# Kernel optimization log

Hardware: AMD Instinct MI355X
Metric: run time of the kernel (lower is better)

Reference implementation:

```python
import jax, jax.numpy as jnp
import numpy as np

D_MODEL = 1024
N_HEADS = 16
D_FF = 4096
LN_EPS = 1e-5


def _layer_norm(x, g, b):
    m = jnp.mean(x, axis=-1, keepdims=True)
    v = jnp.mean((x - m) ** 2, axis=-1, keepdims=True)
    return (x - m) / jnp.sqrt(v + LN_EPS) * g + b


def setup_inputs() -> dict:
    key = jax.random.key(0)
    ks = jax.random.split(key, 16)
    s = 0.02
    d, dff = D_MODEL, D_FF
    return {
        "x": jax.random.normal(ks[0], (8, 1000, d), dtype=jnp.float32),
        # weights stored as (d_in, d_out); applied via x @ W
        "wq": jax.random.normal(ks[1], (d, d), dtype=jnp.float32) * s,
        "wk": jax.random.normal(ks[2], (d, d), dtype=jnp.float32) * s,
        "wv": jax.random.normal(ks[3], (d, d), dtype=jnp.float32) * s,
        "wo": jax.random.normal(ks[4], (d, d), dtype=jnp.float32) * s,
        "bo": jnp.zeros((d,), dtype=jnp.float32),
        "w1": jax.random.normal(ks[5], (d, dff), dtype=jnp.float32) * s,
        "b1": jnp.zeros((dff,), dtype=jnp.float32),
        "w2": jax.random.normal(ks[6], (dff, d), dtype=jnp.float32) * s,
        "b2": jnp.zeros((d,), dtype=jnp.float32),
        "g1": jnp.ones((d,), dtype=jnp.float32),
        "beta1": jnp.zeros((d,), dtype=jnp.float32),
        "g2": jnp.ones((d,), dtype=jnp.float32),
        "beta2": jnp.zeros((d,), dtype=jnp.float32),
    }


def reference(x, wq, wk, wv, wo, bo, w1, b1, w2, b2, g1, beta1, g2, beta2):
    B, S, D = x.shape
    H = N_HEADS
    dk = D // H

    # --- pre-norm attention ---
    h = _layer_norm(x, g1, beta1)
    q = (h @ wq).reshape(B, S, H, dk)
    k = (h @ wk).reshape(B, S, H, dk)
    v = (h @ wv).reshape(B, S, H, dk)
    scores = jnp.einsum('bqhd,bkhd->bhqk', q, k) / jnp.sqrt(jnp.float32(dk))
    mask = jnp.tril(jnp.ones((S, S), dtype=bool))  # causal
    scores = jnp.where(mask, scores, -jnp.inf)
    attn = jax.nn.softmax(scores, axis=-1)
    attended = jnp.einsum('bhqk,bkhd->bqhd', attn, v).reshape(B, S, D)
    x = x + attended @ wo + bo

    # --- pre-norm FFN (exact GELU, matching torch F.gelu default) ---
    h2 = _layer_norm(x, g2, beta2)
    ff = jax.nn.gelu(h2 @ w1 + b1, approximate=False) @ w2 + b2
    return x + ff
```

## Files before the change

kernel.cpp:

```cpp
#include <hip/hip_runtime.h>
#include <hip/hip_bf16.h>
#include <math.h>

#define D_MODEL 1024
#define D_FF    4096
#define N_HEADS 16
#define SEQ     1000
#define BATCH   8
#define M_TOK   (BATCH * SEQ)

typedef __bf16 bf16x8_t __attribute__((ext_vector_type(8)));
typedef short  short8_t __attribute__((ext_vector_type(8)));
typedef float  f32x4_t  __attribute__((ext_vector_type(4)));

__device__ __forceinline__ f32x4_t mfma_bf16(short8_t a, short8_t b, f32x4_t c) {
    return __builtin_amdgcn_mfma_f32_16x16x32_bf16(
        __builtin_bit_cast(bf16x8_t, a), __builtin_bit_cast(bf16x8_t, b), c, 0, 0, 0);
}

__device__ __forceinline__ unsigned short f2bf(float f) {
    union { float f; unsigned u; } x; x.f = f;
    unsigned r = (x.u + 0x7fffu + ((x.u >> 16) & 1u)) >> 16;
    return (unsigned short)r;
}

__device__ __forceinline__ float gelu_fast(float v) {
    float z = 1.5957691216f * v * fmaf(0.044715f, v * v, 1.0f);
    float e = __expf(-z);
    return v * __builtin_amdgcn_rcpf(1.0f + e);
}

__device__ __forceinline__ void gload_lds16(const void* g, void* l) {
    __builtin_amdgcn_global_load_lds(
        (const __attribute__((address_space(1))) unsigned int*)g,
        (__attribute__((address_space(3))) unsigned int*)l, 16, 0, 0);
}

__global__ __launch_bounds__(256) void prep_kernel(
    const float* __restrict__ wq, const float* __restrict__ wk,
    const float* __restrict__ wv, const float* __restrict__ wo,
    const float* __restrict__ w1, const float* __restrict__ w2,
    unsigned short* __restrict__ wqt, unsigned short* __restrict__ wkt,
    unsigned short* __restrict__ wvt, unsigned short* __restrict__ wot,
    unsigned short* __restrict__ w1t, unsigned short* __restrict__ w2t,
    const float* __restrict__ x, const float* __restrict__ g1,
    const float* __restrict__ beta1, unsigned short* __restrict__ h1) {
    int id = blockIdx.x;
    __shared__ float tile[32][33];
    __shared__ float red[8];
    if (id >= 12288) {
        int row = id - 12288, tid = threadIdx.x;
        const float4 v = ((const float4*)(x + (size_t)row * D_MODEL))[tid];
        float s  = v.x + v.y + v.z + v.w;
        float s2 = v.x * v.x + v.y * v.y + v.z * v.z + v.w * v.w;
#pragma unroll
        for (int o = 32; o > 0; o >>= 1) { s += __shfl_xor(s, o, 64); s2 += __shfl_xor(s2, o, 64); }
        int wave = tid >> 6, lane = tid & 63;
        if (lane == 0) { red[wave] = s; red[wave + 4] = s2; }
        __syncthreads();
        s  = red[0] + red[1] + red[2] + red[3];
        s2 = red[4] + red[5] + red[6] + red[7];
        float mean = s * (1.0f / D_MODEL);
        float var  = s2 * (1.0f / D_MODEL) - mean * mean;
        float rstd = rsqrtf(var + 1e-5f);
        float4 gg = ((const float4*)g1)[tid];
        float4 bb = ((const float4*)beta1)[tid];
        ushort4 o4;
        o4.x = f2bf((v.x - mean) * rstd * gg.x + bb.x);
        o4.y = f2bf((v.y - mean) * rstd * gg.y + bb.y);
        o4.z = f2bf((v.z - mean) * rstd * gg.z + bb.z);
        o4.w = f2bf((v.w - mean) * rstd * gg.w + bb.w);
        ((ushort4*)(h1 + (size_t)row * D_MODEL))[tid] = o4;
        return;
    }
    const float* w; unsigned short* wt; int Kd, Nd, bx, by;
    if (id < 4096) {
        int z = id >> 10, t = id & 1023;
        w  = z == 0 ? wq  : z == 1 ? wk  : z == 2 ? wv  : wo;
        wt = z == 0 ? wqt : z == 1 ? wkt : z == 2 ? wvt : wot;
        Kd = 1024; Nd = 1024; bx = t & 31; by = t >> 5;
    } else if (id < 8192) {
        int t = id - 4096;
        w = w1; wt = w1t; Kd = 1024; Nd = 4096; bx = t & 127; by = t >> 7;
    } else {
        int t = id - 8192;
        w = w2; wt = w2t; Kd = 4096; Nd = 1024; bx = t & 31; by = t >> 5;
    }
    int n0 = bx * 32, k0 = by * 32;
    int tx = threadIdx.x & 31, ty = threadIdx.x >> 5;
#pragma unroll
    for (int i = 0; i < 4; ++i)
        tile[ty + i * 8][tx] = w[(size_t)(k0 + ty + i * 8) * Nd + n0 + tx];
    __syncthreads();
#pragma unroll
    for (int i = 0; i < 4; ++i)
        wt[(size_t)(n0 + ty + i * 8) * Kd + k0 + tx] = f2bf(tile[tx][ty + i * 8]);
}

__global__ __launch_bounds__(256) void vtrans_kernel(const unsigned short* __restrict__ v,
                                                     unsigned short* __restrict__ vt) {
    __shared__ unsigned short tile[32][33];
    int b = blockIdx.z;
    int c0 = blockIdx.x * 32, s0 = blockIdx.y * 32;
    int tx = threadIdx.x, ty = threadIdx.y;
#pragma unroll
    for (int i = 0; i < 4; ++i) {
        int s = s0 + ty + i * 8;
        unsigned short val = 0;
        if (s < SEQ) val = v[((size_t)b * SEQ + s) * D_MODEL + c0 + tx];
        tile[ty + i * 8][tx] = val;
    }
    __syncthreads();
#pragma unroll
    for (int i = 0; i < 4; ++i) {
        int c = c0 + ty + i * 8;
        vt[((size_t)b * D_MODEL + c) * 1024 + s0 + tx] = tile[tx][ty + i * 8];
    }
}

__global__ __launch_bounds__(256) void ln_kernel(const float* __restrict__ x,
                                                 const float* __restrict__ g,
                                                 const float* __restrict__ beta,
                                                 unsigned short* __restrict__ out) {
    int row = blockIdx.x, tid = threadIdx.x;
    const float4 v = ((const float4*)(x + (size_t)row * D_MODEL))[tid];
    float s  = v.x + v.y + v.z + v.w;
    float s2 = v.x * v.x + v.y * v.y + v.z * v.z + v.w * v.w;
#pragma unroll
    for (int o = 32; o > 0; o >>= 1) { s += __shfl_xor(s, o, 64); s2 += __shfl_xor(s2, o, 64); }
    __shared__ float red[8];
    int wave = tid >> 6, lane = tid & 63;
    if (lane == 0) { red[wave] = s; red[wave + 4] = s2; }
    __syncthreads();
    s  = red[0] + red[1] + red[2] + red[3];
    s2 = red[4] + red[5] + red[6] + red[7];
    float mean = s * (1.0f / D_MODEL);
    float var  = s2 * (1.0f / D_MODEL) - mean * mean;
    float rstd = rsqrtf(var + 1e-5f);
    float4 gg = ((const float4*)g)[tid];
    float4 bb = ((const float4*)beta)[tid];
    ushort4 o4;
    o4.x = f2bf((v.x - mean) * rstd * gg.x + bb.x);
    o4.y = f2bf((v.y - mean) * rstd * gg.y + bb.y);
    o4.z = f2bf((v.z - mean) * rstd * gg.z + bb.z);
    o4.w = f2bf((v.w - mean) * rstd * gg.w + bb.w);
    ((ushort4*)(out + (size_t)row * D_MODEL))[tid] = o4;
}

enum { EPI_BF16 = 0, EPI_GELU = 1, EPI_RES_F32 = 2 };

template <int EPI, bool FUSE3>
__global__ __launch_bounds__(512, 2) void gemm256(
    const unsigned short* __restrict__ A,
    const unsigned short* __restrict__ Bt0,
    const unsigned short* __restrict__ Bt1,
    const unsigned short* __restrict__ Bt2,
    const float* __restrict__ bias,
    const float* __restrict__ resid,
    void* __restrict__ out0, void* out1, void* out2,
    int Mdim, int Ndim, int K) {
    __shared__ unsigned short lds[4][2][256 * 32];
    int tid = threadIdx.x;
    int lane = tid & 63, wave = tid >> 6;
    int l15 = lane & 15, quad = lane >> 4;
    int wr = wave >> 2;
    int wc = wave & 3;
    int rt = blockIdx.y * 256;
    const unsigned short* Bt = Bt0;
    void* outp = out0;
    int ct;
    if (FUSE3) {
        int sel = blockIdx.x >> 2;
        ct = (blockIdx.x & 3) * 256;
        Bt   = sel == 0 ? Bt0  : (sel == 1 ? Bt1  : Bt2);
        outp = sel == 0 ? out0 : (sel == 1 ? out1 : out2);
    } else {
        ct = blockIdx.x * 256;
    }

    const unsigned short* aS[2];
    const unsigned short* bS[2];
#pragma unroll
    for (int j = 0; j < 2; ++j) {
        int gl = tid + j * 512;
        int p = gl >> 3, slot = gl & 7;
        int sp = slot ^ (p & 7);
        int rrow = 2 * p + (sp >> 2), g2 = sp & 3;
        int ar = rt + rrow; if (ar >= Mdim) ar = Mdim - 1;
        aS[j] = A  + (size_t)ar * K + g2 * 8;
        bS[j] = Bt + (size_t)(ct + rrow) * K + g2 * 8;
    }
    auto stageA = [&](int kt) {
        char* base = (char*)&lds[kt & 3][0][0];
#pragma unroll
        for (int j = 0; j < 2; ++j)
            gload_lds16(aS[j] + (size_t)kt * 32, base + (wave * 64 + j * 512) * 16);
    };
    auto stageB = [&](int kt) {
        char* base = (char*)&lds[kt & 3][1][0];
#pragma unroll
        for (int j = 0; j < 2; ++j)
            gload_lds16(bS[j] + (size_t)kt * 32, base + (wave * 64 + j * 512) * 16);
    };

    int lh = l15 >> 1;
    int mslot = (quad + ((l15 & 1) << 2)) ^ lh;
    unsigned aOff = (unsigned)((wr * 64 + lh) * 128 + mslot * 16);
    unsigned bOff = (unsigned)((wc * 32 + lh) * 128 + mslot * 16);

    f32x4_t acc[8][4] = {};
    int NT = K >> 5;

    stageA(0); stageB(0); stageA(1); stageB(1); stageA(2); stageB(2);

    for (int t = 0; t < NT; ++t) {
        int sl = t & 3;
        int rem = NT - 1 - t;
        if (rem >= 2)      asm volatile("s_waitcnt vmcnt(8)" ::: "memory");
        else if (rem == 1) asm volatile("s_waitcnt vmcnt(4)" ::: "memory");
        else               asm volatile("s_waitcnt vmcnt(0)" ::: "memory");
        __builtin_amdgcn_s_barrier();
        const char* la = (const char*)&lds[sl][0][0];
        const char* lb = (const char*)&lds[sl][1][0];
        short8_t af[4], bfv[4];
#pragma unroll
        for (int mi = 0; mi < 4; ++mi)
            af[mi] = *(const short8_t*)(la + aOff + mi * 1024);
#pragma unroll
        for (int ni = 0; ni < 4; ++ni)
            bfv[ni] = *(const short8_t*)(lb + bOff + ni * 1024);
        if (t + 3 < NT) stageA(t + 3);
        __builtin_amdgcn_s_setprio(1);
#pragma unroll
        for (int mi = 0; mi < 4; ++mi)
#pragma unroll
            for (int ni = 0; ni < 4; ++ni)
                acc[mi][ni] = mfma_bf16(af[mi], bfv[ni], acc[mi][ni]);
        __builtin_amdgcn_s_setprio(0);
        asm volatile("" ::: "memory");
        __builtin_amdgcn_s_barrier();
#pragma unroll
        for (int mi = 0; mi < 4; ++mi)
            af[mi] = *(const short8_t*)(la + aOff + 4096 + mi * 1024);
        if (t + 3 < NT) stageB(t + 3);
        __builtin_amdgcn_s_setprio(1);
#pragma unroll
        for (int mi = 0; mi < 4; ++mi)
#pragma unroll
            for (int ni = 0; ni < 4; ++ni)
                acc[4 + mi][ni] = mfma_bf16(af[mi], bfv[ni], acc[4 + mi][ni]);
        __builtin_amdgcn_s_setprio(0);
    }

    float bias_c[4];
    if (EPI != EPI_BF16) {
#pragma unroll
        for (int ni = 0; ni < 4; ++ni) bias_c[ni] = bias[ct + wc * 64 + ni * 16 + l15];
    }

#pragma unroll
    for (int mi = 0; mi < 8; ++mi) {
#pragma unroll
        for (int r = 0; r < 4; ++r) {
            int grow = rt + wr * 128 + mi * 16 + quad * 4 + r;
            if (grow >= Mdim) continue;
#pragma unroll
            for (int ni = 0; ni < 4; ++ni) {
                int gcol = ct + wc * 64 + ni * 16 + l15;
                float v = acc[mi][ni][r];
                size_t idx = (size_t)grow * Ndim + gcol;
                if (EPI == EPI_BF16) {
                    ((unsigned short*)outp)[idx] = f2bf(v);
                } else if (EPI == EPI_GELU) {
                    v += bias_c[ni];
                    ((unsigned short*)outp)[idx] = f2bf(gelu_fast(v));
                } else {
                    v += bias_c[ni] + resid[idx];
                    ((float*)outp)[idx] = v;
                }
            }
        }
    }
}

template <int EPI, bool FUSE3>
__global__ __launch_bounds__(512, 2) void gemm128(
    const unsigned short* __restrict__ A,
    const unsigned short* __restrict__ Bt0,
    const unsigned short* __restrict__ Bt1,
    const unsigned short* __restrict__ Bt2,
    const float* __restrict__ bias,
    const float* __restrict__ resid,
    void* __restrict__ out0, void* out1, void* out2,
    int Mdim, int Ndim, int K) {
    __shared__ unsigned short ldsA[4][128 * 32];
    __shared__ unsigned short ldsB[4][256 * 32];
    int tid = threadIdx.x;
    int lane = tid & 63, wave = tid >> 6;
    int l15 = lane & 15, quad = lane >> 4;
    int wr = wave >> 2;
    int wc = wave & 3;
    int rt = blockIdx.y * 128;
    const unsigned short* Bt = Bt0;
    void* outp = out0;
    int ct;
    if (FUSE3) {
        int sel = blockIdx.x >> 2;
        ct = (blockIdx.x & 3) * 256;
        Bt   = sel == 0 ? Bt0  : (sel == 1 ? Bt1  : Bt2);
        outp = sel == 0 ? out0 : (sel == 1 ? out1 : out2);
    } else {
        ct = blockIdx.x * 256;
    }

    const unsigned short* aSrc;
    {
        int p = tid >> 3, sp = (tid & 7) ^ (p & 7);
        int rrow = 2 * p + (sp >> 2), g2 = sp & 3;
        int ar = rt + rrow; if (ar >= Mdim) ar = Mdim - 1;
        aSrc = A + (size_t)ar * K + g2 * 8;
    }
    const unsigned short* bSrc[2];
#pragma unroll
    for (int j = 0; j < 2; ++j) {
        int gl = tid + j * 512;
        int p = gl >> 3, sp = (gl & 7) ^ (p & 7);
        int rrow = 2 * p + (sp >> 2), g2 = sp & 3;
        bSrc[j] = Bt + (size_t)(ct + rrow) * K + g2 * 8;
    }
    auto stage = [&](int kt) {
        int sl = kt & 3;
        gload_lds16(aSrc + (size_t)kt * 32, (char*)ldsA[sl] + wave * 1024);
        gload_lds16(bSrc[0] + (size_t)kt * 32, (char*)ldsB[sl] + wave * 1024);
        gload_lds16(bSrc[1] + (size_t)kt * 32, (char*)ldsB[sl] + 8192 + wave * 1024);
    };

    int lh = l15 >> 1;
    int mslot = (quad + ((l15 & 1) << 2)) ^ lh;
    unsigned aOff = (unsigned)((wr * 32 + lh) * 128 + mslot * 16);
    unsigned bOff = (unsigned)((wc * 32 + lh) * 128 + mslot * 16);

    f32x4_t acc[4][4] = {};
    int NT = K >> 5;

    stage(0); stage(1); stage(2);

    for (int t = 0; t < NT; ++t) {
        int sl = t & 3;
        int rem = NT - 1 - t;
        if (rem >= 2)      asm volatile("s_waitcnt vmcnt(6)" ::: "memory");
        else if (rem == 1) asm volatile("s_waitcnt vmcnt(3)" ::: "memory");
        else               asm volatile("s_waitcnt vmcnt(0)" ::: "memory");
        __builtin_amdgcn_s_barrier();
        const char* la = (const char*)ldsA[sl];
        const char* lb = (const char*)ldsB[sl];
        short8_t af[4], bfv[4];
#pragma unroll
        for (int mi = 0; mi < 4; ++mi)
            af[mi] = *(const short8_t*)(la + aOff + mi * 1024);
#pragma unroll
        for (int ni = 0; ni < 4; ++ni)
            bfv[ni] = *(const short8_t*)(lb + bOff + ni * 1024);
        if (t + 3 < NT) stage(t + 3);
        __builtin_amdgcn_s_setprio(1);
#pragma unroll
        for (int mi = 0; mi < 4; ++mi)
#pragma unroll
            for (int ni = 0; ni < 4; ++ni)
                acc[mi][ni] = mfma_bf16(af[mi], bfv[ni], acc[mi][ni]);
        __builtin_amdgcn_s_setprio(0);
    }

    float bias_c[4];
    if (EPI != EPI_BF16) {
#pragma unroll
        for (int ni = 0; ni < 4; ++ni) bias_c[ni] = bias[ct + wc * 64 + ni * 16 + l15];
    }

#pragma unroll
    for (int mi = 0; mi < 4; ++mi) {
#pragma unroll
        for (int r = 0; r < 4; ++r) {
            int grow = rt + wr * 64 + mi * 16 + quad * 4 + r;
            if (grow >= Mdim) continue;
#pragma unroll
            for (int ni = 0; ni < 4; ++ni) {
                int gcol = ct + wc * 64 + ni * 16 + l15;
                float v = acc[mi][ni][r];
                size_t idx = (size_t)grow * Ndim + gcol;
                if (EPI == EPI_BF16) {
                    ((unsigned short*)outp)[idx] = f2bf(v);
                } else if (EPI == EPI_GELU) {
                    v += bias_c[ni];
                    ((unsigned short*)outp)[idx] = f2bf(gelu_fast(v));
                } else {
                    v += bias_c[ni] + resid[idx];
                    ((float*)outp)[idx] = v;
                }
            }
        }
    }
}

__global__ __launch_bounds__(256) void attn_kernel(
    const unsigned short* __restrict__ q,
    const unsigned short* __restrict__ k,
    const unsigned short* __restrict__ vt,
    unsigned short* __restrict__ att) {
    int p = blockIdx.x, h = blockIdx.y, b = blockIdx.z;
    int tid = threadIdx.x, lane = tid & 63, wave = tid >> 6;
    int l15 = lane & 15, quad = lane >> 4;
    __shared__ unsigned short kt_lds[2][64 * 64];
    __shared__ unsigned short vt_lds[2][64 * 64];
    __shared__ unsigned short p_lds[4][32 * 64];
    unsigned short* pw = p_lds[wave];

    const int qtA = p, qtB = 7 - p;
    const int tA = 2 * qtA + 2, tB = 2 * qtB + 2, total = tA + tB;

    short8_t aq[2][2][2];
#pragma unroll
    for (int ph = 0; ph < 2; ++ph) {
        int qw = (ph ? qtB : qtA) * 128 + wave * 32;
#pragma unroll
        for (int g = 0; g < 2; ++g) {
            int qr = qw + g * 16 + l15; if (qr > SEQ - 1) qr = SEQ - 1;
            const unsigned short* qp = q + ((size_t)(b * SEQ + qr)) * D_MODEL + h * 64 + quad * 8;
            aq[ph][g][0] = *(const short8_t*)qp;
            aq[ph][g][1] = *(const short8_t*)(qp + 32);
        }
    }

    f32x4_t o[2][4] = {};
    float m_run[2] = {-3.0e38f, -3.0e38f};
    float l_run[2] = {0.f, 0.f};

    auto stage = [&](int kt, int bufi) {
#pragma unroll
        for (int i = 0; i < 2; ++i) {
            int g2 = tid + i * 256;
            int row = g2 >> 3, cp = g2 & 7;
            int c = cp ^ (row & 7);
            int key = kt * 64 + row; int keyc = key < SEQ ? key : SEQ - 1;
            gload_lds16(k + ((size_t)(b * SEQ + keyc)) * D_MODEL + h * 64 + c * 8,
                        (char*)kt_lds[bufi] + (size_t)(wave * 64 + i * 256) * 16);
            gload_lds16(vt + ((size_t)((b * N_HEADS + h) * 64 + row)) * 1024 + kt * 64 + c * 8,
                        (char*)vt_lds[bufi] + (size_t)(wave * 64 + i * 256) * 16);
        }
    };

    auto flush = [&](int qt) {
#pragma unroll
        for (int g = 0; g < 2; ++g) {
            float linv = __builtin_amdgcn_rcpf(l_run[g]);
#pragma unroll
            for (int r = 0; r < 4; ++r) {
                float nr = __shfl(linv, quad * 4 + r, 64);
                int qg = qt * 128 + wave * 32 + g * 16 + quad * 4 + r;
                if (qg >= SEQ) continue;
#pragma unroll
                for (int db = 0; db < 4; ++db)
                    att[((size_t)(b * SEQ + qg)) * D_MODEL + h * 64 + db * 16 + l15] =
                        f2bf(o[g][db][r] * nr);
            }
        }
#pragma unroll
        for (int g = 0; g < 2; ++g) {
            m_run[g] = -3.0e38f; l_run[g] = 0.f;
#pragma unroll
            for (int db = 0; db < 4; ++db) o[g][db] = f32x4_t{0.f, 0.f, 0.f, 0.f};
        }
    };

    stage(0, 0);

    for (int i = 0; i < total; ++i) {
        int bufi = i & 1;
        __syncthreads();
        if (i + 1 < total) {
            int nkt = (i + 1 < tA) ? (i + 1) : (i + 1 - tA);
            stage(nkt, bufi ^ 1);
        }
        int phase = (i < tA) ? 0 : 1;
        int kt = (i < tA) ? i : i - tA;
        int qt = phase ? qtB : qtA;
        int qw = qt * 128 + wave * 32;
        const unsigned short* kl = kt_lds[bufi];
        const unsigned short* vl = vt_lds[bufi];

        if (kt * 64 <= qw + 31) {
            short8_t kf[4][2];
#pragma unroll
            for (int nb = 0; nb < 4; ++nb)
#pragma unroll
                for (int kc = 0; kc < 2; ++kc) {
                    int row = nb * 16 + l15;
                    kf[nb][kc] = *(const short8_t*)(kl + (row * 8 + ((kc * 4 + quad) ^ (row & 7))) * 8);
                }

            bool gact[2];
#pragma unroll
            for (int g = 0; g < 2; ++g) {
                gact[g] = (kt * 64 <= qw + g * 16 + 15);
                if (!gact[g]) continue;
                f32x4_t s[4] = {};
#pragma unroll
                for (int nb = 0; nb < 4; ++nb)
#pragma unroll
                    for (int kc = 0; kc < 2; ++kc)
                        s[nb] = mfma_bf16(kf[nb][kc], aq[phase][g][kc], s[nb]);
                int qrow = qw + g * 16 + l15;
                float sc[4][4];
#pragma unroll
                for (int nb = 0; nb < 4; ++nb)
#pragma unroll
                    for (int r = 0; r < 4; ++r) {
                        int key = kt * 64 + nb * 16 + quad * 4 + r;
                        float v = s[nb][r] * 0.125f;
                        sc[nb][r] = (key <= qrow) ? v : -1e30f;
                    }
                float mx = sc[0][0];
#pragma unroll
                for (int nb = 0; nb < 4; ++nb)
#pragma unroll
                    for (int r = 0; r < 4; ++r) mx = fmaxf(mx, sc[nb][r]);
                mx = fmaxf(mx, __shfl_xor(mx, 16, 64));
                mx = fmaxf(mx, __shfl_xor(mx, 32, 64));
                float mnew = fmaxf(m_run[g], mx);
                float alpha = __expf(m_run[g] - mnew);
                m_run[g] = mnew;
                float rs = 0.f;
#pragma unroll
                for (int nb = 0; nb < 4; ++nb)
#pragma unroll
                    for (int r = 0; r < 4; ++r) {
                        float pv = __expf(sc[nb][r] - mnew);
                        sc[nb][r] = pv;
                        rs += pv;
                    }
                rs += __shfl_xor(rs, 16, 64);
                rs += __shfl_xor(rs, 32, 64);
                l_run[g] = l_run[g] * alpha + rs;
#pragma unroll
                for (int r = 0; r < 4; ++r) {
                    float a = __shfl(alpha, quad * 4 + r, 64);
#pragma unroll
                    for (int db = 0; db < 4; ++db) o[g][db][r] *= a;
                }
#pragma unroll
                for (int nb = 0; nb < 4; ++nb) {
                    unsigned long long pv =
                        (unsigned long long)f2bf(sc[nb][0]) |
                        ((unsigned long long)f2bf(sc[nb][1]) << 16) |
                        ((unsigned long long)f2bf(sc[nb][2]) << 32) |
                        ((unsigned long long)f2bf(sc[nb][3]) << 48);
                    int chunk = (4 * nb + quad) ^ ((l15 & 7) << 1);
                    *(unsigned long long*)(pw + (g * 16 + l15) * 64 + chunk * 4) = pv;
                }
            }
            asm volatile("s_waitcnt lgkmcnt(0)" ::: "memory");

            short8_t vf[4][2];
#pragma unroll
            for (int db = 0; db < 4; ++db)
#pragma unroll
                for (int kc = 0; kc < 2; ++kc) {
                    int row = db * 16 + l15;
                    vf[db][kc] = *(const short8_t*)(vl + (row * 8 + ((kc * 4 + quad) ^ (row & 7))) * 8);
                }
#pragma unroll
            for (int g = 0; g < 2; ++g) {
                if (!gact[g]) continue;
                short8_t ap[2];
#pragma unroll
                for (int kc = 0; kc < 2; ++kc)
                    ap[kc] = *(const short8_t*)(pw + (g * 16 + l15) * 64 +
                                                ((kc * 4 + quad) ^ (l15 & 7)) * 8);
#pragma unroll
                for (int db = 0; db < 4; ++db)
#pragma unroll
                    for (int kc = 0; kc < 2; ++kc)
                        o[g][db] = mfma_bf16(ap[kc], vf[db][kc], o[g][db]);
            }
        }

        if (i == tA - 1) flush(qtA);
    }
    flush(qtB);
}

extern "C" void kernel_launch(void* const* d_in, const int* in_sizes, int n_in,
                              void* d_out, int out_size, void* d_ws, size_t ws_size,
                              hipStream_t stream) {
    const float* x     = (const float*)d_in[0];
    const float* wq    = (const float*)d_in[1];
    const float* wk    = (const float*)d_in[2];
    const float* wv    = (const float*)d_in[3];
    const float* wo    = (const float*)d_in[4];
    const float* bo    = (const float*)d_in[5];
    const float* w1    = (const float*)d_in[6];
    const float* b1    = (const float*)d_in[7];
    const float* w2    = (const float*)d_in[8];
    const float* b2    = (const float*)d_in[9];
    const float* g1    = (const float*)d_in[10];
    const float* beta1 = (const float*)d_in[11];
    const float* g2    = (const float*)d_in[12];
    const float* beta2 = (const float*)d_in[13];
    float* out = (float*)d_out;
    char* ws = (char*)d_ws;

    const size_t SZ_MD_BF16 = (size_t)M_TOK * D_MODEL * 2;
    unsigned short* h1  = (unsigned short*)(ws);
    unsigned short* qb  = (unsigned short*)(ws + SZ_MD_BF16);
    unsigned short* kb  = (unsigned short*)(ws + 2 * SZ_MD_BF16);
    unsigned short* vb  = (unsigned short*)(ws + 3 * SZ_MD_BF16);
    unsigned short* atb = (unsigned short*)(ws + 4 * SZ_MD_BF16);
    unsigned short* ffb = qb;
    size_t off = 5 * SZ_MD_BF16;
    unsigned short* vtb = (unsigned short*)(ws + off); off += (size_t)BATCH * D_MODEL * 1024 * 2;
    float* x1 = (float*)(ws + off); off += (size_t)M_TOK * D_MODEL * 4;
    unsigned short* wqt = (unsigned short*)(ws + off); off += (size_t)D_MODEL * D_MODEL * 2;
    unsigned short* wkt = (unsigned short*)(ws + off); off += (size_t)D_MODEL * D_MODEL * 2;
    unsigned short* wvt = (unsigned short*)(ws + off); off += (size_t)D_MODEL * D_MODEL * 2;
    unsigned short* wot = (unsigned short*)(ws + off); off += (size_t)D_MODEL * D_MODEL * 2;
    unsigned short* w1t = (unsigned short*)(ws + off); off += (size_t)D_MODEL * D_FF * 2;
    unsigned short* w2t = (unsigned short*)(ws + off); off += (size_t)D_MODEL * D_FF * 2;

    prep_kernel<<<12288 + M_TOK, 256, 0, stream>>>(
        wq, wk, wv, wo, w1, w2, wqt, wkt, wvt, wot, w1t, w2t, x, g1, beta1, h1);

    const int MT128 = (M_TOK + 127) / 128;
    const int MT256 = (M_TOK + 255) / 256;

    gemm128<EPI_BF16, true><<<dim3(12, MT128), 512, 0, stream>>>(
        h1, wqt, wkt, wvt, nullptr, nullptr, qb, kb, vb, M_TOK, D_MODEL, D_MODEL);

    dim3 tb(32, 8);
    vtrans_kernel<<<dim3(32, 32, 8), tb, 0, stream>>>(vb, vtb);

    attn_kernel<<<dim3(4, N_HEADS, BATCH), 256, 0, stream>>>(qb, kb, vtb, atb);

    gemm128<EPI_RES_F32, false><<<dim3(4, MT128), 512, 0, stream>>>(
        atb, wot, nullptr, nullptr, bo, x, x1, nullptr, nullptr, M_TOK, D_MODEL, D_MODEL);

    ln_kernel<<<M_TOK, 256, 0, stream>>>(x1, g2, beta2, h1);

    gemm256<EPI_GELU, false><<<dim3(16, MT256), 512, 0, stream>>>(
        h1, w1t, nullptr, nullptr, b1, nullptr, ffb, nullptr, nullptr, M_TOK, D_FF, D_MODEL);

    gemm128<EPI_RES_F32, false><<<dim3(4, MT128), 512, 0, stream>>>(
        ffb, w2t, nullptr, nullptr, b2, x1, out, nullptr, nullptr, M_TOK, D_MODEL, D_FF);
}
```

Measured before the change: 477.4 us.

## Add 256x256 GEMM with K=64 double buffering and four-phase interleaved pipeline

Replaces the 256-tile GEMM with a version that stages K=64 slices into two LDS buffers and splits each K step into four MFMA phases. Global-to-LDS loads for the next tiles are interleaved between phases, with explicit barriers and sched_barrier calls. The QKV projection moves from 128-row tiles to this 256-row kernel. The aim is to hide load latency and raise MFMA density on the large GEMMs, at the cost of more barriers and a 128KB LDS footprint, which lowers occupancy.

```diff
diff --git a/kernel.cpp b/kernel.cpp
--- a/kernel.cpp
+++ b/kernel.cpp
@@ -149,8 +149,8 @@
 
 enum { EPI_BF16 = 0, EPI_GELU = 1, EPI_RES_F32 = 2 };
 
-template <int EPI, bool FUSE3>
-__global__ __launch_bounds__(512, 2) void gemm256(
+template <int EPI, bool FUSE3, int SLOTS>
+__global__ __launch_bounds__(512, 2) void gemm128t(
     const unsigned short* __restrict__ A,
     const unsigned short* __restrict__ Bt0,
     const unsigned short* __restrict__ Bt1,
@@ -159,7 +159,134 @@
     const float* __restrict__ resid,
     void* __restrict__ out0, void* out1, void* out2,
     int Mdim, int Ndim, int K) {
-    __shared__ unsigned short lds[4][2][256 * 32];
+    constexpr int DIST = SLOTS - 1;
+    __shared__ unsigned short ldsA[SLOTS][128 * 32];
+    __shared__ unsigned short ldsB[SLOTS][256 * 32];
+    int tid = threadIdx.x;
+    int lane = tid & 63, wave = tid >> 6;
+    int l15 = lane & 15, quad = lane >> 4;
+    int wr = wave >> 2;
+    int wc = wave & 3;
+    int rt = blockIdx.y * 128;
+    const unsigned short* Bt = Bt0;
+    void* outp = out0;
+    int ct;
+    if (FUSE3) {
+        int sel = blockIdx.x >> 2;
+        ct = (blockIdx.x & 3) * 256;
+        Bt   = sel == 0 ? Bt0  : (sel == 1 ? Bt1  : Bt2);
+        outp = sel == 0 ? out0 : (sel == 1 ? out1 : out2);
+    } else {
+        ct = blockIdx.x * 256;
+    }
+
+    const unsigned short* aSrc;
+    {
+        int p = tid >> 3, sp = (tid & 7) ^ (p & 7);
+        int rrow = 2 * p + (sp >> 2), g2 = sp & 3;
+        int ar = rt + rrow; if (ar >= Mdim) ar = Mdim - 1;
+        aSrc = A + (size_t)ar * K + g2 * 8;
+    }
+    const unsigned short* bSrc[2];
+#pragma unroll
+    for (int j = 0; j < 2; ++j) {
+        int gl = tid + j * 512;
+        int p = gl >> 3, sp = (gl & 7) ^ (p & 7);
+        int rrow = 2 * p + (sp >> 2), g2 = sp & 3;
+        bSrc[j] = Bt + (size_t)(ct + rrow) * K + g2 * 8;
+    }
+    auto stage = [&](int kt, int sl) {
+        gload_lds16(aSrc + (size_t)kt * 32, (char*)ldsA[sl] + wave * 1024);
+        gload_lds16(bSrc[0] + (size_t)kt * 32, (char*)ldsB[sl] + wave * 1024);
+        gload_lds16(bSrc[1] + (size_t)kt * 32, (char*)ldsB[sl] + 8192 + wave * 1024);
+    };
+
+    int lh = l15 >> 1;
+    int mslot = (quad + ((l15 & 1) << 2)) ^ lh;
+    unsigned aOff = (unsigned)((wr * 32 + lh) * 128 + mslot * 16);
+    unsigned bOff = (unsigned)((wc * 32 + lh) * 128 + mslot * 16);
+
+    f32x4_t acc[4][4] = {};
+    int NT = K >> 5;
+
+#pragma unroll
+    for (int d = 0; d < DIST; ++d) stage(d, d);
+
+    int scur = 0, spre = DIST;
+    for (int t = 0; t < NT; ++t) {
+        int rem = NT - 1 - t;
+        if constexpr (SLOTS == 4) {
+            if (rem >= 2)      asm volatile("s_waitcnt vmcnt(6)" ::: "memory");
+            else if (rem == 1) asm volatile("s_waitcnt vmcnt(3)" ::: "memory");
+            else               asm volatile("s_waitcnt vmcnt(0)" ::: "memory");
+        } else {
+            if (rem >= 1)      asm volatile("s_waitcnt vmcnt(3)" ::: "memory");
+            else               asm volatile("s_waitcnt vmcnt(0)" ::: "memory");
+        }
+        __builtin_amdgcn_s_barrier();
+        const char* la = (const char*)ldsA[scur];
+        const char* lb = (const char*)ldsB[scur];
+        short8_t af[4], bfv[4];
+#pragma unroll
+        for (int mi = 0; mi < 4; ++mi)
+            af[mi] = *(const short8_t*)(la + aOff + mi * 1024);
+#pragma unroll
+        for (int ni = 0; ni < 4; ++ni)
+            bfv[ni] = *(const short8_t*)(lb + bOff + ni * 1024);
+        if (t + DIST < NT) stage(t + DIST, spre);
+        __builtin_amdgcn_s_setprio(1);
+#pragma unroll
+        for (int mi = 0; mi < 4; ++mi)
+#pragma unroll
+            for (int ni = 0; ni < 4; ++ni)
+                acc[mi][ni] = mfma_bf16(af[mi], bfv[ni], acc[mi][ni]);
+        __builtin_amdgcn_s_setprio(0);
+        scur = (scur == SLOTS - 1) ? 0 : scur + 1;
+        spre = (spre == SLOTS - 1) ? 0 : spre + 1;
+    }
+
+    float bias_c[4];
+    if (EPI != EPI_BF16) {
+#pragma unroll
+        for (int ni = 0; ni < 4; ++ni) bias_c[ni] = bias[ct + wc * 64 + ni * 16 + l15];
+    }
+
+#pragma unroll
+    for (int mi = 0; mi < 4; ++mi) {
+#pragma unroll
+        for (int r = 0; r < 4; ++r) {
+            int grow = rt + wr * 64 + mi * 16 + quad * 4 + r;
+            if (grow >= Mdim) continue;
+#pragma unroll
+            for (int ni = 0; ni < 4; ++ni) {
+                int gcol = ct + wc * 64 + ni * 16 + l15;
+                float v = acc[mi][ni][r];
+                size_t idx = (size_t)grow * Ndim + gcol;
+                if (EPI == EPI_BF16) {
+                    ((unsigned short*)outp)[idx] = f2bf(v);
+                } else if (EPI == EPI_GELU) {
+                    v += bias_c[ni];
+                    ((unsigned short*)outp)[idx] = f2bf(gelu_fast(v));
+                } else {
+                    v += bias_c[ni] + resid[idx];
+                    ((float*)outp)[idx] = v;
+                }
+            }
+        }
+    }
+}
+
+template <int EPI, bool FUSE3>
+__global__ __launch_bounds__(512, 2) void gemm256ph(
+    const unsigned short* __restrict__ A,
+    const unsigned short* __restrict__ Bt0,
+    const unsigned short* __restrict__ Bt1,
+    const unsigned short* __restrict__ Bt2,
+    const float* __restrict__ bias,
+    const float* __restrict__ resid,
+    void* __restrict__ out0, void* out1, void* out2,
+    int Mdim, int Ndim, int K) {
+    __shared__ unsigned short lds[2][32768];
     int tid = threadIdx.x;
     int lane = tid & 63, wave = tid >> 6;
     int l15 = lane & 15, quad = lane >> 4;
@@ -178,78 +305,137 @@
         ct = blockIdx.x * 256;
     }
 
-    const unsigned short* aS[2];
-    const unsigned short* bS[2];
+    int r6 = tid >> 3, s8 = tid & 7;
+    int gswA = (s8 ^ (r6 & 7)) * 8;
+    const unsigned short* aP[2][2];
+#pragma unroll
+    for (int j = 0; j < 2; ++j)
+#pragma unroll
+        for (int h = 0; h < 2; ++h) {
+            int ar = rt + j * 128 + h * 64 + r6;
+            if (ar >= Mdim) ar = Mdim - 1;
+            aP[j][h] = A + (size_t)ar * K + gswA;
+        }
+    const unsigned short* bP[2][2];
 #pragma unroll
     for (int j = 0; j < 2; ++j) {
-        int gl = tid + j * 512;
-        int p = gl >> 3, slot = gl & 7;
-        int sp = slot ^ (p & 7);
-        int rrow = 2 * p + (sp >> 2), g2 = sp & 3;
-        int ar = rt + rrow; if (ar >= Mdim) ar = Mdim - 1;
-        aS[j] = A  + (size_t)ar * K + g2 * 8;
-        bS[j] = Bt + (size_t)(ct + rrow) * K + g2 * 8;
-    }
-    auto stageA = [&](int kt) {
-        char* base = (char*)&lds[kt & 3][0][0];
-#pragma unroll
-        for (int j = 0; j < 2; ++j)
-            gload_lds16(aS[j] + (size_t)kt * 32, base + (wave * 64 + j * 512) * 16);
+        int G = tid + j * 512;
+        int q = G >> 8, idx = G & 255;
+        int r5 = idx >> 3, sb = idx & 7;
+        int gswB = (sb ^ (r5 & 7)) * 8;
+#pragma unroll
+        for (int h = 0; h < 2; ++h)
+            bP[j][h] = Bt + (size_t)(ct + q * 64 + h * 32 + r5) * K + gswB;
+    }
+    char* ldsb = (char*)lds;
+    int bwoff = (wave >> 2) * 8192 + (wave & 3) * 1024;
+    auto stA = [&](int kt, int h) {
+        char* d = ldsb + (size_t)(kt & 1) * 65536 + h * 8192 + wave * 1024;
+        gload_lds16(aP[0][h] + (size_t)kt * 64, d);
+        gload_lds16(aP[1][h] + (size_t)kt * 64, d + 16384);
     };
-    auto stageB = [&](int kt) {
-        char* base = (char*)&lds[kt & 3][1][0];
-#pragma unroll
-        for (int j = 0; j < 2; ++j)
-            gload_lds16(bS[j] + (size_t)kt * 32, base + (wave * 64 + j * 512) * 16);
+    auto stB = [&](int kt, int h) {
+        char* d = ldsb + (size_t)(kt & 1) * 65536 + 32768 + h * 4096 + bwoff;
+        gload_lds16(bP[0][h] + (size_t)kt * 64, d);
+        gload_lds16(bP[1][h] + (size_t)kt * 64, d + 16384);
     };
 
-    int lh = l15 >> 1;
-    int mslot = (quad + ((l15 & 1) << 2)) ^ lh;
-    unsigned aOff = (unsigned)((wr * 64 + lh) * 128 + mslot * 16);
-    unsigned bOff = (unsigned)((wc * 32 + lh) * 128 + mslot * 16);
+    unsigned sw0 = (unsigned)((quad ^ (l15 & 7)) * 16);
+    unsigned sw1 = sw0 ^ 64;
+    unsigned aB = (unsigned)(wr * 16384 + l15 * 128);
+    unsigned bB = (unsigned)(32768 + wc * 8192 + l15 * 128);
 
     f32x4_t acc[8][4] = {};
-    int NT = K >> 5;
-
-    stageA(0); stageB(0); stageA(1); stageB(1); stageA(2); stageB(2);
-
-    for (int t = 0; t < NT; ++t) {
-        int sl = t & 3;
-        int rem = NT - 1 - t;
-        if (rem >= 2)      asm volatile("s_waitcnt vmcnt(8)" ::: "memory");
-        else if (rem == 1) asm volatile("s_waitcnt vmcnt(4)" ::: "memory");
-        else               asm volatile("s_waitcnt vmcnt(0)" ::: "memory");
-        __builtin_amdgcn_s_barrier();
-        const char* la = (const char*)&lds[sl][0][0];
-        const char* lb = (const char*)&lds[sl][1][0];
-        short8_t af[4], bfv[4];
+    int NT = K >> 6;
+
+    stA(0, 0); stB(0, 0); stA(0, 1); stB(0, 1);
+    stA(1, 0); stB(1, 0); stA(1, 1);
+    asm volatile("s_waitcnt vmcnt(6)" ::: "memory");
+    __builtin_amdgcn_s_barrier();
+
+    short8_t af[4][2], bf[4][2];
+    for (int kt = 0; kt < NT; ++kt) {
+        const char* sbase = ldsb + (size_t)(kt & 1) * 65536;
+#pragma unroll
+        for (int mi = 0; mi < 4; ++mi) {
+            af[mi][0] = *(const short8_t*)(sbase + aB + sw0 + mi * 2048);
+            af[mi][1] = *(const short8_t*)(sbase + aB + sw1 + mi * 2048);
+        }
+#pragma unroll
+        for (int ni = 0; ni < 2; ++ni) {
+            bf[ni][0] = *(const short8_t*)(sbase + bB + sw0 + ni * 2048);
+            bf[ni][1] = *(const short8_t*)(sbase + bB + sw1 + ni * 2048);
+        }
+        if (kt + 1 < NT) stB(kt + 1, 1);
+        __builtin_amdgcn_s_barrier();
+        asm volatile("s_waitcnt lgkmcnt(0)" ::: "memory");
+        __builtin_amdgcn_sched_barrier(0);
+        __builtin_amdgcn_s_setprio(1);
 #pragma unroll
         for (int mi = 0; mi < 4; ++mi)
-            af[mi] = *(const short8_t*)(la + aOff + mi * 1024);
-#pragma unroll
-        for (int ni = 0; ni < 4; ++ni)
-            bfv[ni] = *(const short8_t*)(lb + bOff + ni * 1024);
-        if (t + 3 < NT) stageA(t + 3);
+#pragma unroll
+            for (int ni = 0; ni < 2; ++ni) {
+                acc[mi][ni] = mfma_bf16(af[mi][0], bf[ni][0], acc[mi][ni]);
+                acc[mi][ni] = mfma_bf16(af[mi][1], bf[ni][1], acc[mi][ni]);
+            }
+        __builtin_amdgcn_s_setprio(0);
+        __builtin_amdgcn_s_barrier();
+#pragma unroll
+        for (int ni = 2; ni < 4; ++ni) {
+            bf[ni][0] = *(const short8_t*)(sbase + bB + sw0 + ni * 2048);
+            bf[ni][1] = *(const short8_t*)(sbase + bB + sw1 + ni * 2048);
+        }
+        if (kt + 2 < NT) stA(kt + 2, 0);
+        __builtin_amdgcn_s_barrier();
+        asm volatile("s_waitcnt lgkmcnt(0)" ::: "memory");
+        __builtin_amdgcn_sched_barrier(0);
         __builtin_amdgcn_s_setprio(1);
 #pragma unroll
         for (int mi = 0; mi < 4; ++mi)
 #pragma unroll
-            for (int ni = 0; ni < 4; ++ni)
-                acc[mi][ni] = mfma_bf16(af[mi], bfv[ni], acc[mi][ni]);
+            for (int ni = 2; ni < 4; ++ni) {
+                acc[mi][ni] = mfma_bf16(af[mi][0], bf[ni][0], acc[mi][ni]);
+                acc[mi][ni] = mfma_bf16(af[mi][1], bf[ni][1], acc[mi][ni]);
+            }
         __builtin_amdgcn_s_setprio(0);
-        asm volatile("" ::: "memory");
-        __builtin_amdgcn_s_barrier();
+        __builtin_amdgcn_s_barrier();
+#pragma unroll
+        for (int mi = 0; mi < 4; ++mi) {
+            af[mi][0] = *(const short8_t*)(sbase + aB + sw0 + (mi + 4) * 2048);
+            af[mi][1] = *(const short8_t*)(sbase + aB + sw1 + (mi + 4) * 2048);
+        }
+        if (kt + 2 < NT) stB(kt + 2, 0);
+        __builtin_amdgcn_s_barrier();
+        asm volatile("s_waitcnt lgkmcnt(0)" ::: "memory");
+        __builtin_amdgcn_sched_barrier(0);
+        __builtin_amdgcn_s_setprio(1);
 #pragma unroll
         for (int mi = 0; mi < 4; ++mi)
-            af[mi] = *(const short8_t*)(la + aOff + 4096 + mi * 1024);
-        if (t + 3 < NT) stageB(t + 3);
+#pragma unroll
+            for (int ni = 2; ni < 4; ++ni) {
+                acc[mi + 4][ni] = mfma_bf16(af[mi][0], bf[ni][0], acc[mi + 4][ni]);
+                acc[mi + 4][ni] = mfma_bf16(af[mi][1], bf[ni][1], acc[mi + 4][ni]);
+            }
+        __builtin_amdgcn_s_setprio(0);
+        __builtin_amdgcn_s_barrier();
+        if (kt + 2 < NT) {
+            stA(kt + 2, 1);
+            asm volatile("s_waitcnt vmcnt(6)" ::: "memory");
+        } else {
+            asm volatile("s_waitcnt vmcnt(0)" ::: "memory");
+        }
+        __builtin_amdgcn_s_barrier();
+        __builtin_amdgcn_sched_barrier(0);
         __builtin_amdgcn_s_setprio(1);
 #pragma unroll
         for (int mi = 0; mi < 4; ++mi)
 #pragma unroll
-            for (int ni = 0; ni < 4; ++ni)
-                acc[4 + mi][ni] = mfma_bf16(af[mi], bfv[ni], acc[4 + mi][ni]);
+            for (int ni = 0; ni < 2; ++ni) {
+                acc[mi + 4][ni] = mfma_bf16(af[mi][0], bf[ni][0], acc[mi + 4][ni]);
+                acc[mi + 4][ni] = mfma_bf16(af[mi][1], bf[ni][1], acc[mi + 4][ni]);
+            }
         __builtin_amdgcn_s_setprio(0);
+        __builtin_amdgcn_s_barrier();
     }
 
     float bias_c[4];
@@ -263,125 +449,6 @@
 #pragma unroll
         for (int r = 0; r < 4; ++r) {
             int grow = rt + wr * 128 + mi * 16 + quad * 4 + r;
-            if (grow >= Mdim) continue;
-#pragma unroll
-            for (int ni = 0; ni < 4; ++ni) {
-                int gcol = ct + wc * 64 + ni * 16 + l15;
-                float v = acc[mi][ni][r];
-                size_t idx = (size_t)grow * Ndim + gcol;
-                if (EPI == EPI_BF16) {
-                    ((unsigned short*)outp)[idx] = f2bf(v);
-                } else if (EPI == EPI_GELU) {
-                    v += bias_c[ni];
-                    ((unsigned short*)outp)[idx] = f2bf(gelu_fast(v));
-                } else {
-                    v += bias_c[ni] + resid[idx];
-                    ((float*)outp)[idx] = v;
-                }
-            }
-        }
-    }
-}
-
-template <int EPI, bool FUSE3>
-__global__ __launch_bounds__(512, 2) void gemm128(
-    const unsigned short* __restrict__ A,
-    const unsigned short* __restrict__ Bt0,
-    const unsigned short* __restrict__ Bt1,
-    const unsigned short* __restrict__ Bt2,
-    const float* __restrict__ bias,
-    const float* __restrict__ resid,
-    void* __restrict__ out0, void* out1, void* out2,
-    int Mdim, int Ndim, int K) {
-    __shared__ unsigned short ldsA[4][128 * 32];
-    __shared__ unsigned short ldsB[4][256 * 32];
-    int tid = threadIdx.x;
-    int lane = tid & 63, wave = tid >> 6;
-    int l15 = lane & 15, quad = lane >> 4;
-    int wr = wave >> 2;
-    int wc = wave & 3;
-    int rt = blockIdx.y * 128;
-    const unsigned short* Bt = Bt0;
-    void* outp = out0;
-    int ct;
-    if (FUSE3) {
-        int sel = blockIdx.x >> 2;
-        ct = (blockIdx.x & 3) * 256;
-        Bt   = sel == 0 ? Bt0  : (sel == 1 ? Bt1  : Bt2);
-        outp = sel == 0 ? out0 : (sel == 1 ? out1 : out2);
-    } else {
-        ct = blockIdx.x * 256;
-    }
-
-    const unsigned short* aSrc;
-    {
-        int p = tid >> 3, sp = (tid & 7) ^ (p & 7);
-        int rrow = 2 * p + (sp >> 2), g2 = sp & 3;
-        int ar = rt + rrow; if (ar >= Mdim) ar = Mdim - 1;
-        aSrc = A + (size_t)ar * K + g2 * 8;
-    }
-    const unsigned short* bSrc[2];
-#pragma unroll
-    for (int j = 0; j < 2; ++j) {
-        int gl = tid + j * 512;
-        int p = gl >> 3, sp = (gl & 7) ^ (p & 7);
-        int rrow = 2 * p + (sp >> 2), g2 = sp & 3;
-        bSrc[j] = Bt + (size_t)(ct + rrow) * K + g2 * 8;
-    }
-    auto stage = [&](int kt) {
-        int sl = kt & 3;
-        gload_lds16(aSrc + (size_t)kt * 32, (char*)ldsA[sl] + wave * 1024);
-        gload_lds16(bSrc[0] + (size_t)kt * 32, (char*)ldsB[sl] + wave * 1024);
-        gload_lds16(bSrc[1] + (size_t)kt * 32, (char*)ldsB[sl] + 8192 + wave * 1024);
-    };
-
-    int lh = l15 >> 1;
-    int mslot = (quad + ((l15 & 1) << 2)) ^ lh;
-    unsigned aOff = (unsigned)((wr * 32 + lh) * 128 + mslot * 16);
-    unsigned bOff = (unsigned)((wc * 32 + lh) * 128 + mslot * 16);
-
-    f32x4_t acc[4][4] = {};
-    int NT = K >> 5;
-
-    stage(0); stage(1); stage(2);
-
-    for (int t = 0; t < NT; ++t) {
-        int sl = t & 3;
-        int rem = NT - 1 - t;
-        if (rem >= 2)      asm volatile("s_waitcnt vmcnt(6)" ::: "memory");
-        else if (rem == 1) asm volatile("s_waitcnt vmcnt(3)" ::: "memory");
-        else               asm volatile("s_waitcnt vmcnt(0)" ::: "memory");
-        __builtin_amdgcn_s_barrier();
-        const char* la = (const char*)ldsA[sl];
-        const char* lb = (const char*)ldsB[sl];
-        short8_t af[4], bfv[4];
-#pragma unroll
-        for (int mi = 0; mi < 4; ++mi)
-            af[mi] = *(const short8_t*)(la + aOff + mi * 1024);
-#pragma unroll
-        for (int ni = 0; ni < 4; ++ni)
-            bfv[ni] = *(const short8_t*)(lb + bOff + ni * 1024);
-        if (t + 3 < NT) stage(t + 3);
-        __builtin_amdgcn_s_setprio(1);
-#pragma unroll
-        for (int mi = 0; mi < 4; ++mi)
-#pragma unroll
-            for (int ni = 0; ni < 4; ++ni)
-                acc[mi][ni] = mfma_bf16(af[mi], bfv[ni], acc[mi][ni]);
-        __builtin_amdgcn_s_setprio(0);
-    }
-
-    float bias_c[4];
-    if (EPI != EPI_BF16) {
-#pragma unroll
-        for (int ni = 0; ni < 4; ++ni) bias_c[ni] = bias[ct + wc * 64 + ni * 16 + l15];
-    }
-
-#pragma unroll
-    for (int mi = 0; mi < 4; ++mi) {
-#pragma unroll
-        for (int r = 0; r < 4; ++r) {
-            int grow = rt + wr * 64 + mi * 16 + quad * 4 + r;
             if (grow >= Mdim) continue;
 #pragma unroll
             for (int ni = 0; ni < 4; ++ni) {
@@ -632,7 +699,7 @@
     const int MT128 = (M_TOK + 127) / 128;
     const int MT256 = (M_TOK + 255) / 256;
 
-    gemm128<EPI_BF16, true><<<dim3(12, MT128), 512, 0, stream>>>(
+    gemm256ph<EPI_BF16, true><<<dim3(12, MT256), 512, 0, stream>>>(
         h1, wqt, wkt, wvt, nullptr, nullptr, qb, kb, vb, M_TOK, D_MODEL, D_MODEL);
 
     dim3 tb(32, 8);
@@ -640,14 +707,14 @@
 
     attn_kernel<<<dim3(4, N_HEADS, BATCH), 256, 0, stream>>>(qb, kb, vtb, atb);
 
-    gemm128<EPI_RES_F32, false><<<dim3(4, MT128), 512, 0, stream>>>(
+    gemm128t<EPI_RES_F32, false, 4><<<dim3(4, MT128), 512, 0, stream>>>(
         atb, wot, nullptr, nullptr, bo, x, x1, nullptr, nullptr, M_TOK, D_MODEL, D_MODEL);
 
     ln_kernel<<<M_TOK, 256, 0, stream>>>(x1, g2, beta2, h1);
 
-    gemm256<EPI_GELU, false><<<dim3(16, MT256), 512, 0, stream>>>(
+    gemm256ph<EPI_GELU, false><<<dim3(16, MT256), 512, 0, stream>>>(
         h1, w1t, nullptr, nullptr, b1, nullptr, ffb, nullptr, nullptr, M_TOK, D_FF, D_MODEL);
 
-    gemm128<EPI_RES_F32, false><<<dim3(4, MT128), 512, 0, stream>>>(
+    gemm128t<EPI_RES_F32, false, 4><<<dim3(4, MT128), 512, 0, stream>>>(
         ffb, w2t, nullptr, nullptr, b2, x1, out, nullptr, nullptr, M_TOK, D_MODEL, D_FF);
 }
```

Result: no change. 472.6 us (-1.0%).
